# Kernel optimization log

Measured on AMD Instinct MI355X. Metric: run time of the kernel, lower is better.

Reference implementation:

```python
import jax, jax.numpy as jnp
import numpy as np

N_NODES = 65536
N_EDGES = 1048576
IN_FEATS = 128
H1 = 128
H2 = 256
N_CLASSES = 16


def setup_inputs() -> dict:
    key = jax.random.key(0)
    ks = jax.random.split(key, 12)
    s = 0.05
    x = jax.random.normal(ks[0], (N_NODES, IN_FEATS), dtype=jnp.float32)
    src = jax.random.randint(ks[1], (N_EDGES,), 0, N_NODES, dtype=jnp.int32)
    dst = jax.random.randint(ks[2], (N_EDGES,), 0, N_NODES, dtype=jnp.int32)
    # SAGEConv('pool') params: fc_pool (bias), fc_self (no bias), fc_neigh (no bias), output bias
    Wp = jax.random.normal(ks[3], (H1, IN_FEATS), dtype=jnp.float32) * s
    bp = jnp.zeros((H1,), dtype=jnp.float32)
    Ws = jax.random.normal(ks[4], (H1, IN_FEATS), dtype=jnp.float32) * s
    Wn = jax.random.normal(ks[5], (H1, H1), dtype=jnp.float32) * s
    bn = jnp.zeros((H1,), dtype=jnp.float32)
    # MLP head
    W1 = jax.random.normal(ks[6], (H2, H1), dtype=jnp.float32) * s
    b1 = jnp.zeros((H2,), dtype=jnp.float32)
    W2 = jax.random.normal(ks[7], (N_CLASSES, H2), dtype=jnp.float32) * s
    b2 = jnp.zeros((N_CLASSES,), dtype=jnp.float32)
    return {"x": x, "Wp": Wp, "bp": bp, "Ws": Ws, "Wn": Wn, "bn": bn,
            "W1": W1, "b1": b1, "W2": W2, "b2": b2, "src": src, "dst": dst}


def reference(x, Wp, bp, Ws, Wn, bn, W1, b1, W2, b2, src, dst):
    N = x.shape[0]
    # SAGEConv 'pool': per-edge MLP on gathered source features, segment-max over dst
    m = jax.nn.relu(x[src] @ Wp.T + bp)              # [E, H1]
    pooled = jax.ops.segment_max(m, dst, num_segments=N)  # [N, H1], -inf for isolated
    pooled = jnp.where(jnp.isneginf(pooled), 0.0, pooled)
    h = x @ Ws.T + pooled @ Wn.T + bn                # combine self + neigh
    h = jax.nn.leaky_relu(h)                         # slope 0.01 matches torch default
    h = jax.nn.leaky_relu(h @ W1.T + b1)
    # dropout is identity in eval mode
    h = jax.nn.sigmoid(h @ W2.T + b2)
    return h
```

## Files before the change

### kernel.cpp

```cpp
#include <hip/hip_runtime.h>
#include <cstdint>
#include <cstddef>

typedef __attribute__((ext_vector_type(8))) __bf16 bf16x8;
typedef __attribute__((ext_vector_type(4))) float f32x4;

union bf8pack { unsigned short u[8]; bf16x8 v; uint4 q; };

#define BCAP 768

static __device__ __forceinline__ unsigned short f2b(float f) {
    union { float f; unsigned int u; } v; v.f = f;
    unsigned int u = v.u;
    unsigned int r = (u + 0x7fffu + ((u >> 16) & 1u)) >> 16;
    return (unsigned short)r;
}

static __device__ __forceinline__ bf16x8 cvt8(const float* __restrict__ p) {
    float4 f0 = *(const float4*)p;
    float4 f1 = *(const float4*)(p + 4);
    bf8pack pk;
    pk.u[0] = f2b(f0.x); pk.u[1] = f2b(f0.y);
    pk.u[2] = f2b(f0.z); pk.u[3] = f2b(f0.w);
    pk.u[4] = f2b(f1.x); pk.u[5] = f2b(f1.y);
    pk.u[6] = f2b(f1.z); pk.u[7] = f2b(f1.w);
    return pk.v;
}

static __device__ __forceinline__ unsigned int pkmax(unsigned int a, unsigned int b) {
    unsigned int d;
    asm("v_pk_max_u16 %0, %1, %2" : "=v"(d) : "v"(a), "v"(b));
    return d;
}

__global__ __launch_bounds__(256) void mega0(
    const int* __restrict__ src, const int* __restrict__ dst,
    int* __restrict__ bcnt, unsigned int* __restrict__ pairs,
    const float* __restrict__ x, const float* __restrict__ Wp,
    const float* __restrict__ bp,
    const float* __restrict__ Ws, const float* __restrict__ Wn,
    const float* __restrict__ W1, const float* __restrict__ W2,
    unsigned short* __restrict__ Wcat, unsigned short* __restrict__ W1_b,
    unsigned short* __restrict__ W2_b, unsigned short* __restrict__ y,
    unsigned short* __restrict__ xb)
{
    const int tid = threadIdx.x;
    const int bx = (int)blockIdx.x;

    if (bx >= 768) {
        int i = (bx - 768) * 256 + tid;
        if (i < 32768) {
            int o = i >> 8, k = i & 255;
            Wcat[i] = f2b(k < 128 ? Ws[o * 128 + k] : Wn[o * 128 + (k - 128)]);
        } else if (i < 65536) {
            W1_b[i - 32768] = f2b(W1[i - 32768]);
        } else {
            W2_b[i - 65536] = f2b(W2[i - 65536]);
        }
        return;
    }

    if (bx >= 256) {
        const int bm = bx - 256;
        const int w  = tid >> 6;
        const int wm = w & 1, wn = w >> 1;
        const int l  = tid & 63;
        const int lr = l & 15, quad = l >> 4;
        const int m0 = bm * 128 + wm * 64;
        const int n0 = wn * 64;

        f32x4 acc[4][4];
#pragma unroll
        for (int i = 0; i < 4; i++)
#pragma unroll
            for (int j = 0; j < 4; j++) acc[i][j] = (f32x4){0.f, 0.f, 0.f, 0.f};

        const float* Apf = x  + (size_t)(m0 + lr) * 128 + quad * 8;
        const float* Bpf = Wp + (size_t)(n0 + lr) * 128 + quad * 8;

#pragma unroll
        for (int ks = 0; ks < 4; ks++) {
            bf16x8 af[4], bf[4];
#pragma unroll
            for (int i = 0; i < 4; i++) {
                const float* p = Apf + (size_t)i * 16 * 128 + ks * 32;
                float4 f0 = *(const float4*)p;
                float4 f1 = *(const float4*)(p + 4);
                bf8pack pk;
                pk.u[0] = f2b(f0.x); pk.u[1] = f2b(f0.y);
                pk.u[2] = f2b(f0.z); pk.u[3] = f2b(f0.w);
                pk.u[4] = f2b(f1.x); pk.u[5] = f2b(f1.y);
                pk.u[6] = f2b(f1.z); pk.u[7] = f2b(f1.w);
                af[i] = pk.v;
                if (wn == 0)
                    *(uint4*)(xb + (size_t)(m0 + lr + i * 16) * 128 + ks * 32 + quad * 8) = pk.q;
            }
#pragma unroll
            for (int i = 0; i < 4; i++)
                bf[i] = cvt8(Bpf + (size_t)i * 16 * 128 + ks * 32);
#pragma unroll
            for (int mi = 0; mi < 4; mi++)
#pragma unroll
                for (int ni = 0; ni < 4; ni++)
                    acc[mi][ni] = __builtin_amdgcn_mfma_f32_16x16x32_bf16(
                        af[mi], bf[ni], acc[mi][ni], 0, 0, 0);
        }

#pragma unroll
        for (int ni = 0; ni < 4; ni++) {
            const int col = n0 + ni * 16 + lr;
            const float bv = bp[col];
#pragma unroll
            for (int mi = 0; mi < 4; mi++) {
#pragma unroll
                for (int r = 0; r < 4; r++) {
                    const int row = m0 + mi * 16 + quad * 4 + r;
                    float v = acc[mi][ni][r] + bv;
                    v = v > 0.f ? v : 0.f;
                    y[(size_t)row * 128 + col] = f2b(v);
                }
            }
        }
        return;
    }

    __shared__ int h[2048];
    __shared__ int base_l[2048];
    __shared__ int cnt[2048];
    for (int i = tid; i < 2048; i += 256) { h[i] = 0; cnt[i] = 0; }
    __syncthreads();
    const int base = bx * 4096;
    int d_r[16], s_r[16];
    const int4* s4 = (const int4*)(src + base);
    const int4* d4 = (const int4*)(dst + base);
#pragma unroll
    for (int i = 0; i < 4; i++) {
        int4 dv = d4[tid + i * 256];
        int4 sv = s4[tid + i * 256];
        d_r[i * 4 + 0] = dv.x; d_r[i * 4 + 1] = dv.y;
        d_r[i * 4 + 2] = dv.z; d_r[i * 4 + 3] = dv.w;
        s_r[i * 4 + 0] = sv.x; s_r[i * 4 + 1] = sv.y;
        s_r[i * 4 + 2] = sv.z; s_r[i * 4 + 3] = sv.w;
    }
#pragma unroll
    for (int i = 0; i < 16; i++)
        atomicAdd(&h[((unsigned)d_r[i]) >> 5], 1);
    __syncthreads();
    for (int i = tid; i < 2048; i += 256)
        base_l[i] = h[i] ? (i * BCAP + atomicAdd(&bcnt[i], h[i])) : 0;
    __syncthreads();
#pragma unroll
    for (int i = 0; i < 16; i++) {
        int b = ((unsigned)d_r[i]) >> 5;
        int pos = base_l[b] + atomicAdd(&cnt[b], 1);
        if (pos < (b + 1) * BCAP)
            pairs[pos] = ((unsigned)s_r[i] << 5) | ((unsigned)d_r[i] & 31u);
    }
}

__global__ __launch_bounds__(256, 4) void megaB(
    const unsigned int* __restrict__ yu, const int* __restrict__ bcnt,
    const unsigned int* __restrict__ pairs,
    const unsigned short* __restrict__ xb,
    const unsigned short* __restrict__ Wcat, const float* __restrict__ bn,
    const unsigned short* __restrict__ W1_b, const float* __restrict__ b1,
    const unsigned short* __restrict__ W2_b, const float* __restrict__ b2,
    float* __restrict__ out)
{
    __shared__ unsigned short S[32 * 264];
    __shared__ unsigned short ldsSrc[1024];
    __shared__ int bin[32], offl[32], cnt2[32];
    unsigned int* PS = (unsigned int*)&S[32 * 136];

    const int b = blockIdx.x;
    const int tid = threadIdx.x;
    const int w = tid >> 6, l = tid & 63;
    const int lr = l & 15, quad = l >> 4;
    const int row0 = b * 32;

    if (tid < 32) { bin[tid] = 0; cnt2[tid] = 0; }
    __syncthreads();
    const int beg = b * BCAP;
    int nb = bcnt[b]; nb = nb < BCAP ? nb : BCAP;

    for (int i = tid; i < nb; i += 256)
        atomicAdd(&bin[pairs[beg + i] & 31u], 1);
    __syncthreads();

    if (tid < 32) {
        int c = bin[tid];
        int p = (c + 7) & ~7;
        int s = p;
#pragma unroll
        for (int d = 1; d < 32; d <<= 1) {
            int t = __shfl_up(s, d);
            if (tid >= d) s += t;
        }
        offl[tid] = s - p;
    }
    __syncthreads();

    for (int i = tid; i < nb; i += 256) {
        unsigned int p = pairs[beg + i];
        int d = p & 31u;
        int slot = offl[d] + atomicAdd(&cnt2[d], 1);
        ldsSrc[slot] = (unsigned short)(p >> 5);
    }
    __syncthreads();

    if (tid < 32) {
        int c = bin[tid];
        if (c > 0) {
            int o = offl[tid];
            unsigned short last = ldsSrc[o + c - 1];
            int p = (c + 7) & ~7;
            for (int k = c; k < p; k++) ldsSrc[o + k] = last;
        }
    }
    __syncthreads();

    const unsigned int* __restrict__ ylane = yu + l;
#pragma unroll
    for (int g = 0; g < 2; g++) {
        const int n0 = w * 8 + g * 4;
        unsigned int acc[4] = {0u, 0u, 0u, 0u};
        int e0a[4], rka[4];
#pragma unroll
        for (int k = 0; k < 4; k++) {
            e0a[k] = offl[n0 + k];
            rka[k] = (bin[n0 + k] + 7) >> 3;
        }
        int maxr = rka[0];
#pragma unroll
        for (int k = 1; k < 4; k++) maxr = rka[k] > maxr ? rka[k] : maxr;

        for (int r = 0; r < maxr; r++) {
            unsigned int vv[4][8];
#pragma unroll
            for (int k = 0; k < 4; k++) {
                if (r < rka[k]) {
                    uint4 sv = *(const uint4*)&ldsSrc[e0a[k] + r * 8];
                    vv[k][0] = ylane[(size_t)(sv.x & 0xffffu) << 6];
                    vv[k][1] = ylane[(size_t)(sv.x >> 16) << 6];
                    vv[k][2] = ylane[(size_t)(sv.y & 0xffffu) << 6];
                    vv[k][3] = ylane[(size_t)(sv.y >> 16) << 6];
                    vv[k][4] = ylane[(size_t)(sv.z & 0xffffu) << 6];
                    vv[k][5] = ylane[(size_t)(sv.z >> 16) << 6];
                    vv[k][6] = ylane[(size_t)(sv.w & 0xffffu) << 6];
                    vv[k][7] = ylane[(size_t)(sv.w >> 16) << 6];
                }
            }
#pragma unroll
            for (int k = 0; k < 4; k++) {
                if (r < rka[k]) {
                    unsigned int m01 = pkmax(vv[k][0], vv[k][1]);
                    unsigned int m23 = pkmax(vv[k][2], vv[k][3]);
                    unsigned int m45 = pkmax(vv[k][4], vv[k][5]);
                    unsigned int m67 = pkmax(vv[k][6], vv[k][7]);
                    acc[k] = pkmax(acc[k], pkmax(pkmax(m01, m23), pkmax(m45, m67)));
                }
            }
        }
#pragma unroll
        for (int k = 0; k < 4; k++) {
            const int n = n0 + k;
            PS[n * 64 + (l ^ ((n & 7) << 2))] = acc[k];
        }
    }
    __syncthreads();

    {
        f32x4 acc[2][2];
#pragma unroll
        for (int i = 0; i < 2; i++)
#pragma unroll
            for (int j = 0; j < 2; j++) acc[i][j] = (f32x4){0.f, 0.f, 0.f, 0.f};

        const unsigned short* Axp = xb + (size_t)(row0 + lr) * 128 + quad * 8;
        const unsigned short* Bp = Wcat + (size_t)(w * 32 + lr) * 256 + quad * 8;

#pragma unroll
        for (int ks = 0; ks < 8; ks++) {
            bf16x8 af[2], bf[2];
            if (ks < 4) {
#pragma unroll
                for (int i = 0; i < 2; i++)
                    af[i] = *(const bf16x8*)(Axp + (size_t)i * 16 * 128 + ks * 32);
            } else {
#pragma unroll
                for (int i = 0; i < 2; i++) {
                    const int row = i * 16 + lr;
                    const int c0 = (ks - 4) * 16 + quad * 4;
                    af[i] = *(const bf16x8*)&PS[row * 64 + (c0 ^ ((row & 7) << 2))];
                }
            }
#pragma unroll
            for (int i = 0; i < 2; i++)
                bf[i] = *(const bf16x8*)(Bp + (size_t)i * 16 * 256 + ks * 32);
#pragma unroll
            for (int mi = 0; mi < 2; mi++)
#pragma unroll
                for (int ni = 0; ni < 2; ni++)
                    acc[mi][ni] = __builtin_amdgcn_mfma_f32_16x16x32_bf16(
                        af[mi], bf[ni], acc[mi][ni], 0, 0, 0);
        }

#pragma unroll
        for (int ni = 0; ni < 2; ni++) {
            const int col = w * 32 + ni * 16 + lr;
            const float bv = bn[col];
#pragma unroll
            for (int mi = 0; mi < 2; mi++) {
#pragma unroll
                for (int r = 0; r < 4; r++) {
                    const int row = mi * 16 + quad * 4 + r;
                    float v = acc[mi][ni][r] + bv;
                    v = v > 0.f ? v : 0.01f * v;
                    S[row * 136 + col] = f2b(v);
                }
            }
        }
    }
    __syncthreads();

    {
        f32x4 acc[2][4];
#pragma unroll
        for (int i = 0; i < 2; i++)
#pragma unroll
            for (int j = 0; j < 4; j++) acc[i][j] = (f32x4){0.f, 0.f, 0.f, 0.f};

        const unsigned short* Bp = W1_b + (size_t)(w * 64 + lr) * 128 + quad * 8;

#pragma unroll
        for (int ks = 0; ks < 4; ks++) {
            bf16x8 af[2], bfr[4];
#pragma unroll
            for (int i = 0; i < 2; i++)
                af[i] = *(const bf16x8*)&S[(i * 16 + lr) * 136 + ks * 32 + quad * 8];
#pragma unroll
            for (int i = 0; i < 4; i++)
                bfr[i] = *(const bf16x8*)(Bp + (size_t)i * 16 * 128 + ks * 32);
#pragma unroll
            for (int mi = 0; mi < 2; mi++)
#pragma unroll
                for (int ni = 0; ni < 4; ni++)
                    acc[mi][ni] = __builtin_amdgcn_mfma_f32_16x16x32_bf16(
                        af[mi], bfr[ni], acc[mi][ni], 0, 0, 0);
        }
        __syncthreads();

#pragma unroll
        for (int ni = 0; ni < 4; ni++) {
            const int col = w * 64 + ni * 16 + lr;
            const float bv = b1[col];
#pragma unroll
            for (int mi = 0; mi < 2; mi++) {
#pragma unroll
                for (int r = 0; r < 4; r++) {
                    const int row = mi * 16 + quad * 4 + r;
                    float v = acc[mi][ni][r] + bv;
                    v = v > 0.f ? v : 0.01f * v;
                    S[row * 264 + col] = f2b(v);
                }
            }
        }
    }
    __syncthreads();

    if (w < 2) {
        const int m0 = w * 16;
        f32x4 a2 = (f32x4){0.f, 0.f, 0.f, 0.f};
#pragma unroll
        for (int ks = 0; ks < 8; ks++) {
            bf16x8 a = *(const bf16x8*)&S[(m0 + lr) * 264 + ks * 32 + quad * 8];
            bf16x8 bb = *(const bf16x8*)(W2_b + (size_t)lr * 256 + ks * 32 + quad * 8);
            a2 = __builtin_amdgcn_mfma_f32_16x16x32_bf16(a, bb, a2, 0, 0, 0);
        }
        const float bv = b2[lr];
#pragma unroll
        for (int r = 0; r < 4; r++) {
            const int row = row0 + m0 + quad * 4 + r;
            float v = a2[r] + bv;
            out[(size_t)row * 16 + lr] = 1.f / (1.f + __expf(-v));
        }
    }
}

extern "C" void kernel_launch(void* const* d_in, const int* in_sizes, int n_in,
                              void* d_out, int out_size, void* d_ws, size_t ws_size,
                              hipStream_t stream)
{
    const float* x  = (const float*)d_in[0];
    const float* Wp = (const float*)d_in[1];
    const float* bp = (const float*)d_in[2];
    const float* Ws = (const float*)d_in[3];
    const float* Wn = (const float*)d_in[4];
    const float* bn = (const float*)d_in[5];
    const float* W1 = (const float*)d_in[6];
    const float* b1 = (const float*)d_in[7];
    const float* W2 = (const float*)d_in[8];
    const float* b2 = (const float*)d_in[9];
    const int* src  = (const int*)d_in[10];
    const int* dst  = (const int*)d_in[11];
    float* out = (float*)d_out;

    const int N = in_sizes[0] / 128;

    unsigned short* y    = (unsigned short*)d_ws;
    unsigned short* xb   = (unsigned short*)((char*)d_ws + (size_t)16 * 1024 * 1024);
    unsigned short* Wcat = (unsigned short*)((char*)d_ws + (size_t)32 * 1024 * 1024);
    unsigned short* W1_b = Wcat + 32768;
    unsigned short* W2_b = W1_b + 32768;
    int* bcnt = (int*)(W2_b + 4096);
    unsigned int* pairs = (unsigned int*)(bcnt + 2048);

    dim3 blk(256);

    hipMemsetAsync(bcnt, 0, 2048 * sizeof(int), stream);

    mega0<<<1040, blk, 0, stream>>>(src, dst, bcnt, pairs,
                                    x, Wp, bp, Ws, Wn, W1, W2,
                                    Wcat, W1_b, W2_b, y, xb);

    megaB<<<N / 32, blk, 0, stream>>>((const unsigned int*)y, bcnt, pairs,
                                      xb, Wcat, bn, W1_b, b1, W2_b, b2, out);
}
```

Measured before the change: 205.4 us.

## Replace global-atomic bucket scatter with per-block fixed slots and byte counts

The edge binning stops reserving space in each destination bucket through global atomics. Each scatter block now writes into its own fixed 24-entry slot per bucket and records a byte count, which removes the global atomic pass and the memset. The consumer kernel reads 256 counts, computes offsets with a prefix scan, and compacts the chunks into LDS before binning. The cost is more scattered small reads in the consumer, a larger pairs buffer, and edges silently dropped if a block sends more than 24 edges to one bucket or a bucket receives more than 1024.

```diff
diff --git a/kernel.cpp b/kernel.cpp
--- a/kernel.cpp
+++ b/kernel.cpp
@@ -7,7 +7,8 @@
 
 union bf8pack { unsigned short u[8]; bf16x8 v; uint4 q; };
 
-#define BCAP 768
+#define SCAP 24
+#define NSB  256
 
 static __device__ __forceinline__ unsigned short f2b(float f) {
     union { float f; unsigned int u; } v; v.f = f;
@@ -35,7 +36,7 @@
 
 __global__ __launch_bounds__(256) void mega0(
     const int* __restrict__ src, const int* __restrict__ dst,
-    int* __restrict__ bcnt, unsigned int* __restrict__ pairs,
+    unsigned char* __restrict__ cnts8, unsigned int* __restrict__ pairs,
     const float* __restrict__ x, const float* __restrict__ Wp,
     const float* __restrict__ bp,
     const float* __restrict__ Ws, const float* __restrict__ Wn,
@@ -124,10 +125,8 @@
         return;
     }
 
-    __shared__ int h[2048];
-    __shared__ int base_l[2048];
     __shared__ int cnt[2048];
-    for (int i = tid; i < 2048; i += 256) { h[i] = 0; cnt[i] = 0; }
+    for (int i = tid; i < 2048; i += 256) cnt[i] = 0;
     __syncthreads();
     const int base = bx * 4096;
     int d_r[16], s_r[16];
@@ -143,23 +142,23 @@
         s_r[i * 4 + 2] = sv.z; s_r[i * 4 + 3] = sv.w;
     }
 #pragma unroll
-    for (int i = 0; i < 16; i++)
-        atomicAdd(&h[((unsigned)d_r[i]) >> 5], 1);
-    __syncthreads();
-    for (int i = tid; i < 2048; i += 256)
-        base_l[i] = h[i] ? (i * BCAP + atomicAdd(&bcnt[i], h[i])) : 0;
-    __syncthreads();
-#pragma unroll
     for (int i = 0; i < 16; i++) {
         int b = ((unsigned)d_r[i]) >> 5;
-        int pos = base_l[b] + atomicAdd(&cnt[b], 1);
-        if (pos < (b + 1) * BCAP)
-            pairs[pos] = ((unsigned)s_r[i] << 5) | ((unsigned)d_r[i] & 31u);
+        int idx = atomicAdd(&cnt[b], 1);
+        if (idx < SCAP)
+            pairs[((size_t)b * NSB + bx) * SCAP + idx] =
+                ((unsigned)s_r[i] << 5) | ((unsigned)d_r[i] & 31u);
+    }
+    __syncthreads();
+    for (int i = tid; i < 2048; i += 256) {
+        int c = cnt[i]; c = c < SCAP ? c : SCAP;
+        cnts8[(size_t)bx * 2048 + i] = (unsigned char)c;
     }
 }
 
 __global__ __launch_bounds__(256, 4) void megaB(
-    const unsigned int* __restrict__ yu, const int* __restrict__ bcnt,
+    const unsigned int* __restrict__ yu,
+    const unsigned char* __restrict__ cnts8,
     const unsigned int* __restrict__ pairs,
     const unsigned short* __restrict__ xb,
     const unsigned short* __restrict__ Wcat, const float* __restrict__ bn,
@@ -168,8 +167,10 @@
     float* __restrict__ out)
 {
     __shared__ unsigned short S[32 * 264];
+    __shared__ unsigned int ldsTmp[1024];
     __shared__ unsigned short ldsSrc[1024];
     __shared__ int bin[32], offl[32], cnt2[32];
+    __shared__ int wtot[4];
     unsigned int* PS = (unsigned int*)&S[32 * 136];
 
     const int b = blockIdx.x;
@@ -179,29 +180,42 @@
     const int row0 = b * 32;
 
     if (tid < 32) { bin[tid] = 0; cnt2[tid] = 0; }
-    __syncthreads();
-    const int beg = b * BCAP;
-    int nb = bcnt[b]; nb = nb < BCAP ? nb : BCAP;
+
+    int c = cnts8[(size_t)tid * 2048 + b];
+    int s = c;
+#pragma unroll
+    for (int d = 1; d < 64; d <<= 1) { int t = __shfl_up(s, d); if (l >= d) s += t; }
+    if (l == 63) wtot[w] = s;
+    __syncthreads();
+    int woff = 0;
+#pragma unroll
+    for (int k = 0; k < 4; k++) woff += (k < w) ? wtot[k] : 0;
+    const int off = woff + s - c;
+    const int nb = wtot[0] + wtot[1] + wtot[2] + wtot[3];
+    const unsigned int* chunk = pairs + ((size_t)b * NSB + tid) * SCAP;
+    for (int j = 0; j < c; j++)
+        if (off + j < 1024) ldsTmp[off + j] = chunk[j];
+    __syncthreads();
 
     for (int i = tid; i < nb; i += 256)
-        atomicAdd(&bin[pairs[beg + i] & 31u], 1);
+        atomicAdd(&bin[ldsTmp[i] & 31u], 1);
     __syncthreads();
 
     if (tid < 32) {
-        int c = bin[tid];
-        int p = (c + 7) & ~7;
-        int s = p;
+        int cc = bin[tid];
+        int p = (cc + 7) & ~7;
+        int ss = p;
 #pragma unroll
         for (int d = 1; d < 32; d <<= 1) {
-            int t = __shfl_up(s, d);
-            if (tid >= d) s += t;
-        }
-        offl[tid] = s - p;
+            int t = __shfl_up(ss, d);
+            if (tid >= d) ss += t;
+        }
+        offl[tid] = ss - p;
     }
     __syncthreads();
 
     for (int i = tid; i < nb; i += 256) {
-        unsigned int p = pairs[beg + i];
+        unsigned int p = ldsTmp[i];
         int d = p & 31u;
         int slot = offl[d] + atomicAdd(&cnt2[d], 1);
         ldsSrc[slot] = (unsigned short)(p >> 5);
@@ -209,12 +223,12 @@
     __syncthreads();
 
     if (tid < 32) {
-        int c = bin[tid];
-        if (c > 0) {
+        int cc = bin[tid];
+        if (cc > 0) {
             int o = offl[tid];
-            unsigned short last = ldsSrc[o + c - 1];
-            int p = (c + 7) & ~7;
-            for (int k = c; k < p; k++) ldsSrc[o + k] = last;
+            unsigned short last = ldsSrc[o + cc - 1];
+            int p = (cc + 7) & ~7;
+            for (int k = cc; k < p; k++) ldsSrc[o + k] = last;
         }
     }
     __syncthreads();
@@ -412,17 +426,15 @@
     unsigned short* Wcat = (unsigned short*)((char*)d_ws + (size_t)32 * 1024 * 1024);
     unsigned short* W1_b = Wcat + 32768;
     unsigned short* W2_b = W1_b + 32768;
-    int* bcnt = (int*)(W2_b + 4096);
-    unsigned int* pairs = (unsigned int*)(bcnt + 2048);
+    unsigned char* cnts8 = (unsigned char*)(W2_b + 4096);
+    unsigned int* pairs  = (unsigned int*)(cnts8 + (size_t)NSB * 2048);
 
     dim3 blk(256);
 
-    hipMemsetAsync(bcnt, 0, 2048 * sizeof(int), stream);
-
-    mega0<<<1040, blk, 0, stream>>>(src, dst, bcnt, pairs,
+    mega0<<<1040, blk, 0, stream>>>(src, dst, cnts8, pairs,
                                     x, Wp, bp, Ws, Wn, W1, W2,
                                     Wcat, W1_b, W2_b, y, xb);
 
-    megaB<<<N / 32, blk, 0, stream>>>((const unsigned int*)y, bcnt, pairs,
+    megaB<<<N / 32, blk, 0, stream>>>((const unsigned int*)y, cnts8, pairs,
                                       xb, Wcat, bn, W1_b, b1, W2_b, b2, out);
 }
```

After: 216.3 us. +5.3%, slower.
